# Performance work log

Measured on AMD Instinct MI355X. Metric: run time of the kernel, lower is better.

The kernel has to match this reference:

```python
import jax, jax.numpy as jnp
import numpy as np

NU, NI = 100000, 50000
N = NU + NI
CU, CI = 100, 100
D = 64
NL = 3
NNZ = 4_000_000
CNNZ = 5000
B = 4096


def setup_inputs() -> dict:
    key = jax.random.key(0)
    ks = jax.random.split(key, 24)
    def edges(k1, k2, k3, nnz, n):
        return (jax.random.randint(k1, (nnz,), 0, n, dtype=jnp.int32),
                jax.random.randint(k2, (nnz,), 0, n, dtype=jnp.int32),
                jax.random.uniform(k3, (nnz,), dtype=jnp.float32) * 0.05)
    ar, ac, av = edges(ks[0], ks[1], ks[2], NNZ, N)
    s1r, s1c, s1v = edges(ks[3], ks[4], ks[5], NNZ, N)
    s2r, s2c, s2v = edges(ks[6], ks[7], ks[8], NNZ, N)
    cr, cc, cv = edges(ks[9], ks[10], ks[11], CNNZ, CU + CI)
    return {
        "user_emb": jax.random.normal(ks[12], (NU, D), dtype=jnp.float32) * 0.1,
        "item_emb": jax.random.normal(ks[13], (NI, D), dtype=jnp.float32) * 0.1,
        "adj_rows": ar, "adj_cols": ac, "adj_vals": av,
        "sg1_rows": s1r, "sg1_cols": s1c, "sg1_vals": s1v,
        "sg2_rows": s2r, "sg2_cols": s2c, "sg2_vals": s2v,
        "uc": jax.random.uniform(ks[14], (NU, CU), dtype=jnp.float32),
        "ic": jax.random.uniform(ks[15], (NI, CI), dtype=jnp.float32),
        "cg_rows": cr, "cg_cols": cc, "cg_vals": cv,
        "users": jax.random.randint(ks[16], (B,), 0, NU, dtype=jnp.int32),
        "items": jax.random.randint(ks[17], (B,), 0, NI, dtype=jnp.int32),
        "neg_items": jax.random.randint(ks[18], (B,), 0, NI, dtype=jnp.int32),
    }


def _gcn(rows, cols, vals, ego, n):
    """n_layers of SpMM propagation + mean over layer outputs (incl. layer 0)."""
    acc = ego
    x = ego
    for _ in range(NL):
        x = jax.ops.segment_sum(vals[:, None] * x[cols], rows, num_segments=n)
        acc = acc + x
    return acc / (NL + 1)


def reference(user_emb, item_emb,
              adj_rows, adj_cols, adj_vals,
              sg1_rows, sg1_cols, sg1_vals,
              sg2_rows, sg2_cols, sg2_vals,
              uc, ic, cg_rows, cg_cols, cg_vals,
              users, items, neg_items):
    ego = jnp.concatenate([user_emb, item_emb], axis=0)  # [N, D]
    e0 = _gcn(adj_rows, adj_cols, adj_vals, ego, N)
    e1 = _gcn(sg1_rows, sg1_cols, sg1_vals, ego, N)
    e2 = _gcn(sg2_rows, sg2_cols, sg2_vals, ego, N)
    # community GCN: project node embeddings onto community space, propagate, lift back
    ucf = uc.T @ user_emb                                # [CU, D]
    icf = ic.T @ item_emb                                # [CI, D]
    ec = _gcn(cg_rows, cg_cols, cg_vals,
              jnp.concatenate([ucf, icf], axis=0), CU + CI)
    u3 = uc @ ec[:CU]                                    # [NU, D]
    i3 = ic @ ec[CU:]                                    # [NI, D]
    user_f = jnp.concatenate([e0[:NU], e1[:NU], e2[:NU], u3], axis=1)  # [NU, 4D]
    item_f = jnp.concatenate([e0[NU:], e1[NU:], e2[NU:], i3], axis=1)  # [NI, 4D]
    ue = user_f[users]
    ie = item_f[items]
    ne = item_f[neg_items]
    # sup_logits = <u, i_pos> - <u, i_neg>
    return jnp.sum(ue * (ie - ne), axis=-1)
```

## Files before the change

kernel.cpp:

```cpp
#include <hip/hip_runtime.h>
#include <hip/hip_fp16.h>
#include <cstdint>
#include <cstddef>

#define NU_ 100000
#define NI_ 50000
#define NN_ 150000
#define D_  64
#define NNZ_ 4000000
#define CN_ 200
#define CNNZ_ 5000
#define B_ 4096

#define NB2   512
#define RPB2  293
#define SLICE 40
#define NBLK  512
#define ECAP  8448

#define NP    4
#define COLP  37500
#define HSZ   (RPB2 * NP)

#define PROJB 1024

#define VSC_   256.0f

#if defined(__has_builtin)
#if __has_builtin(__builtin_amdgcn_cvt_scalef32_pk_f32_fp4) && \
    __has_builtin(__builtin_amdgcn_cvt_scalef32_pk_fp4_f32)
#define USE_FP4 1
#endif
#endif
#ifndef USE_FP4
#define USE_FP4 0
#endif

#if USE_FP4
#define FSC0 8.0f
#define FSC1 32.0f
#define FSC2 512.0f
#define ROWB 32
#else
#define FSC0 32.0f
#define FSC1 32.0f
#define FSC2 32.0f
#define ROWB 64
#endif

typedef float v2f __attribute__((ext_vector_type(2)));
typedef int   v4i __attribute__((ext_vector_type(4)));
typedef float v4f __attribute__((ext_vector_type(4)));

__device__ __forceinline__ float cv8(unsigned char b) {
    return __builtin_amdgcn_cvt_f32_fp8((int)b, 0);
}


#if USE_FP4
__global__ __launch_bounds__(256) void k_toq(const float* __restrict__ a,
                                             const float* __restrict__ b,
                                             unsigned* __restrict__ dst) {
    size_t gid = (size_t)blockIdx.x * 256 + threadIdx.x;
    size_t off = gid * 8;
    if (off >= (size_t)NN_ * D_) return;
    const float* src = (off < (size_t)NU_ * D_) ? a + off : b + (off - (size_t)NU_ * D_);
    float4 f0 = *(const float4*)src;
    float4 f1 = *(const float4*)(src + 4);
    unsigned w = 0;
    w = __builtin_amdgcn_cvt_scalef32_pk_fp4_f32(w, f0.x * FSC0, f0.y * FSC0, 1.0f, 0);
    w = __builtin_amdgcn_cvt_scalef32_pk_fp4_f32(w, f0.z * FSC0, f0.w * FSC0, 1.0f, 1);
    w = __builtin_amdgcn_cvt_scalef32_pk_fp4_f32(w, f1.x * FSC0, f1.y * FSC0, 1.0f, 2);
    w = __builtin_amdgcn_cvt_scalef32_pk_fp4_f32(w, f1.z * FSC0, f1.w * FSC0, 1.0f, 3);
    dst[gid] = w;
}
#else
__global__ __launch_bounds__(256) void k_toq(const float* __restrict__ a,
                                             const float* __restrict__ b,
                                             unsigned* __restrict__ dst) {
    size_t gid = (size_t)blockIdx.x * 256 + threadIdx.x;
    size_t off = gid * 4;
    if (off >= (size_t)NN_ * D_) return;
    const float* src = (off < (size_t)NU_ * D_) ? a + off : b + (off - (size_t)NU_ * D_);
    float4 f = *(const float4*)src;
    int p = 0;
    p = __builtin_amdgcn_cvt_pk_fp8_f32(f.x * FSC0, f.y * FSC0, p, false);
    p = __builtin_amdgcn_cvt_pk_fp8_f32(f.z * FSC0, f.w * FSC0, p, true);
    dst[gid] = (unsigned)p;
}
#endif


__global__ __launch_bounds__(256) void k_bin(const int* __restrict__ rows,
                                             const int* __restrict__ cols,
                                             const float* __restrict__ vals,
                                             int* __restrict__ bcnt,
                                             int2* __restrict__ gbuf) {
    __shared__ int lcur[NB2];
    int t = threadIdx.x;
    for (int i = t; i < NB2; i += 256) lcur[i] = 0;
    __syncthreads();
    size_t blockbase = (size_t)blockIdx.x * NB2 * SLICE;

    for (int base = blockIdx.x * 1024; base < NNZ_; base += gridDim.x * 1024) {
        int i0 = base + t * 4;
        if (i0 < NNZ_) {
            v4i r4 = __builtin_nontemporal_load((const v4i*)(rows + i0));
            v4i c4 = __builtin_nontemporal_load((const v4i*)(cols + i0));
            v4f v4 = __builtin_nontemporal_load((const v4f*)(vals + i0));
            #pragma unroll
            for (int k = 0; k < 4; k++) {
                int r = (k == 0) ? r4.x : (k == 1) ? r4.y : (k == 2) ? r4.z : r4.w;
                int c = (k == 0) ? c4.x : (k == 1) ? c4.y : (k == 2) ? c4.z : c4.w;
                float v = (k == 0) ? v4.x : (k == 1) ? v4.y : (k == 2) ? v4.z : v4.w;
                int b  = r / RPB2;
                int rl = r - b * RPB2;
                int pos = atomicAdd(&lcur[b], 1);
                if (pos < SLICE)
                    gbuf[blockbase + (size_t)b * SLICE + pos] =
                        make_int2((rl << 18) | c, __float_as_int(v));
            }
        }
    }
    __syncthreads();
    for (int i = t; i < NB2; i += 256)
        bcnt[(size_t)blockIdx.x * NB2 + i] = min(lcur[i], SLICE);
}


__global__ void k_btot(const int* __restrict__ bcnt, int* __restrict__ btot) {
    __shared__ int s[256];
    int b = blockIdx.x, t = threadIdx.x;
    int sum = 0;
    for (int sl = t; sl < NBLK; sl += 256) sum += bcnt[(size_t)sl * NB2 + b];
    s[t] = sum;
    __syncthreads();
    for (int o = 128; o > 0; o >>= 1) {
        if (t < o) s[t] += s[t + o];
        __syncthreads();
    }
    if (t == 0) btot[b] = s[0];
}

__global__ void k_bscan(const int* __restrict__ btot, int* __restrict__ bbase,
                        int* __restrict__ row_ptr) {
    __shared__ int s[NB2];
    int t = threadIdx.x;
    int v = btot[t];
    s[t] = v;
    __syncthreads();
    for (int o = 1; o < NB2; o <<= 1) {
        int x = (t >= o) ? s[t - o] : 0;
        __syncthreads();
        s[t] += x;
        __syncthreads();
    }
    bbase[t] = s[t] - v;
    if (t == NB2 - 1) row_ptr[NN_] = s[t];
}


__global__ __launch_bounds__(1024) void k_csr(const int* __restrict__ bcnt,
                                              const int2* __restrict__ gbuf,
                                              const int* __restrict__ bbase,
                                              const int* __restrict__ btot,
                                              int* __restrict__ row_ptr,
                                              unsigned* __restrict__ ep) {
    __shared__ int h[HSZ];
    __shared__ int hx[HSZ];
    __shared__ int aux[1024];
    __shared__ unsigned estage[ECAP];
    int b = blockIdx.x, t = threadIdx.x;
    for (int i = t; i < HSZ; i += 1024) h[i] = 0;
    __syncthreads();

    int sl = t >> 1, part = t & 1;
    int n = bcnt[(size_t)sl * NB2 + b];
    const int2* src = gbuf + ((size_t)sl * NB2 + b) * SLICE;

    for (int i = part; i < n; i += 2) {
        unsigned xv = *(const unsigned*)(src + i);
        int rl = xv >> 18;
        int pnl = (int)(xv & 0x3FFFFu) / COLP;
        atomicAdd(&h[rl * NP + pnl], 1);
    }
    __syncthreads();

    int a0 = (2 * t     < HSZ) ? h[2 * t]     : 0;
    int a1 = (2 * t + 1 < HSZ) ? h[2 * t + 1] : 0;
    aux[t] = a0 + a1;
    __syncthreads();
    for (int o = 1; o < 1024; o <<= 1) {
        int x = (t >= o) ? aux[t - o] : 0;
        __syncthreads();
        aux[t] += x;
        __syncthreads();
    }
    int excl = t ? aux[t - 1] : 0;
    if (2 * t     < HSZ) hx[2 * t]     = excl;
    if (2 * t + 1 < HSZ) hx[2 * t + 1] = excl + a0;
    __syncthreads();

    int base = bbase[b];
    int r0 = b * RPB2;
    int rows_b = min(RPB2, NN_ - r0);
    for (int i = t; i < rows_b; i += 1024) row_ptr[r0 + i] = base + hx[i * NP];
    __syncthreads();

    for (int i = part; i < n; i += 2) {
        int2 e = src[i];
        unsigned ex = (unsigned)e.x;
        int rl = ex >> 18;
        unsigned c = ex & 0x3FFFFu;
        int pnl = (int)c / COLP;
        float v = __int_as_float(e.y) * VSC_;
        unsigned v8 = (unsigned)__builtin_amdgcn_cvt_pk_fp8_f32(v, 0.f, 0, false) & 0xFFu;
        int pos = atomicAdd(&hx[rl * NP + pnl], 1);
        if (pos < ECAP) estage[pos] = c | (v8 << 24);
    }
    __syncthreads();

    int total = btot[b];
    if (total > ECAP) total = ECAP;
    for (int i = t; i < total; i += 1024) ep[base + i] = estage[i];
}


__global__ __launch_bounds__(256) void k_spmm(const int* __restrict__ rp,
                                              const unsigned* __restrict__ ep,
                                              const unsigned char* __restrict__ xq,
                                              float finsc,
                                              unsigned char* __restrict__ xn) {
    int w = (blockIdx.x * 256 + threadIdx.x) >> 6;
    if (w >= NN_) return;
    int lane = threadIdx.x & 63;
    int oct = lane >> 3;
    int l8  = lane & 7;
    int j0 = rp[w], j1 = rp[w + 1];
    v2f a01 = {0.f, 0.f}, a23 = {0.f, 0.f}, a45 = {0.f, 0.f}, a67 = {0.f, 0.f};
    #pragma unroll 4
    for (int j = j0; j < j1; j += 8) {
        int je = j + oct;
        unsigned e = (je < j1) ? ep[je] : 0u;
        float v = __builtin_amdgcn_cvt_f32_fp8((int)e, 3);
        v2f vv = {v, v};
#if USE_FP4
        unsigned raw = *(const unsigned*)(xq + (size_t)(e & 0x3FFFFu) * 32 + l8 * 4);
        a01 += vv * __builtin_amdgcn_cvt_scalef32_pk_f32_fp4(raw, 1.0f, 0);
        a23 += vv * __builtin_amdgcn_cvt_scalef32_pk_f32_fp4(raw, 1.0f, 1);
        a45 += vv * __builtin_amdgcn_cvt_scalef32_pk_f32_fp4(raw, 1.0f, 2);
        a67 += vv * __builtin_amdgcn_cvt_scalef32_pk_f32_fp4(raw, 1.0f, 3);
#else
        uint2 raw = *(const uint2*)(xq + (size_t)(e & 0x3FFFFu) * 64 + l8 * 8);
        a01 += vv * __builtin_amdgcn_cvt_pk_f32_fp8((int)raw.x, false);
        a23 += vv * __builtin_amdgcn_cvt_pk_f32_fp8((int)raw.x, true);
        a45 += vv * __builtin_amdgcn_cvt_pk_f32_fp8((int)raw.y, false);
        a67 += vv * __builtin_amdgcn_cvt_pk_f32_fp8((int)raw.y, true);
#endif
    }
    float d0 = a01[0], d1 = a01[1], d2 = a23[0], d3 = a23[1];
    float d4 = a45[0], d5 = a45[1], d6 = a67[0], d7 = a67[1];
    #pragma unroll
    for (int o = 32; o >= 8; o >>= 1) {
        d0 += __shfl_xor(d0, o, 64); d1 += __shfl_xor(d1, o, 64);
        d2 += __shfl_xor(d2, o, 64); d3 += __shfl_xor(d3, o, 64);
        d4 += __shfl_xor(d4, o, 64); d5 += __shfl_xor(d5, o, 64);
        d6 += __shfl_xor(d6, o, 64); d7 += __shfl_xor(d7, o, 64);
    }
    if (lane < 8) {
#if USE_FP4
        unsigned o2 = 0;
        o2 = __builtin_amdgcn_cvt_scalef32_pk_fp4_f32(o2, d0 * finsc, d1 * finsc, 1.0f, 0);
        o2 = __builtin_amdgcn_cvt_scalef32_pk_fp4_f32(o2, d2 * finsc, d3 * finsc, 1.0f, 1);
        o2 = __builtin_amdgcn_cvt_scalef32_pk_fp4_f32(o2, d4 * finsc, d5 * finsc, 1.0f, 2);
        o2 = __builtin_amdgcn_cvt_scalef32_pk_fp4_f32(o2, d6 * finsc, d7 * finsc, 1.0f, 3);
        *(unsigned*)(xn + (size_t)w * 32 + l8 * 4) = o2;
#else
        int p0 = 0, p1 = 0;
        p0 = __builtin_amdgcn_cvt_pk_fp8_f32(d0 * finsc, d1 * finsc, p0, false);
        p0 = __builtin_amdgcn_cvt_pk_fp8_f32(d2 * finsc, d3 * finsc, p0, true);
        p1 = __builtin_amdgcn_cvt_pk_fp8_f32(d4 * finsc, d5 * finsc, p1, false);
        p1 = __builtin_amdgcn_cvt_pk_fp8_f32(d6 * finsc, d7 * finsc, p1, true);
        uint2 o2; o2.x = (unsigned)p0; o2.y = (unsigned)p1;
        *(uint2*)(xn + (size_t)w * 64 + l8 * 8) = o2;
#endif
    }
}


__global__ __launch_bounds__(256) void k_spmm_s(const int* __restrict__ rp,
                                                const unsigned* __restrict__ ep,
                                                const unsigned char* __restrict__ xq,
                                                float finsc,
                                                const int* __restrict__ users,
                                                const int* __restrict__ items,
                                                const int* __restrict__ negs,
                                                float* __restrict__ x3s) {
    int s = (blockIdx.x * 256 + threadIdx.x) >> 6;
    if (s >= 3 * B_) return;
    int lane = threadIdx.x & 63;
    int oct = lane >> 3;
    int l8  = lane & 7;
    int node;
    if (s < B_)          node = users[s];
    else if (s < 2 * B_) node = NU_ + items[s - B_];
    else                 node = NU_ + negs[s - 2 * B_];
    int j0 = rp[node], j1 = rp[node + 1];
    v2f a01 = {0.f, 0.f}, a23 = {0.f, 0.f}, a45 = {0.f, 0.f}, a67 = {0.f, 0.f};
    #pragma unroll 2
    for (int j = j0; j < j1; j += 8) {
        int je = j + oct;
        unsigned e = (je < j1) ? ep[je] : 0u;
        float v = __builtin_amdgcn_cvt_f32_fp8((int)e, 3);
        v2f vv = {v, v};
#if USE_FP4
        unsigned raw = *(const unsigned*)(xq + (size_t)(e & 0x3FFFFu) * 32 + l8 * 4);
        a01 += vv * __builtin_amdgcn_cvt_scalef32_pk_f32_fp4(raw, 1.0f, 0);
        a23 += vv * __builtin_amdgcn_cvt_scalef32_pk_f32_fp4(raw, 1.0f, 1);
        a45 += vv * __builtin_amdgcn_cvt_scalef32_pk_f32_fp4(raw, 1.0f, 2);
        a67 += vv * __builtin_amdgcn_cvt_scalef32_pk_f32_fp4(raw, 1.0f, 3);
#else
        uint2 raw = *(const uint2*)(xq + (size_t)(e & 0x3FFFFu) * 64 + l8 * 8);
        a01 += vv * __builtin_amdgcn_cvt_pk_f32_fp8((int)raw.x, false);
        a23 += vv * __builtin_amdgcn_cvt_pk_f32_fp8((int)raw.x, true);
        a45 += vv * __builtin_amdgcn_cvt_pk_f32_fp8((int)raw.y, false);
        a67 += vv * __builtin_amdgcn_cvt_pk_f32_fp8((int)raw.y, true);
#endif
    }
    float d0 = a01[0], d1 = a01[1], d2 = a23[0], d3 = a23[1];
    float d4 = a45[0], d5 = a45[1], d6 = a67[0], d7 = a67[1];
    #pragma unroll
    for (int o = 32; o >= 8; o >>= 1) {
        d0 += __shfl_xor(d0, o, 64); d1 += __shfl_xor(d1, o, 64);
        d2 += __shfl_xor(d2, o, 64); d3 += __shfl_xor(d3, o, 64);
        d4 += __shfl_xor(d4, o, 64); d5 += __shfl_xor(d5, o, 64);
        d6 += __shfl_xor(d6, o, 64); d7 += __shfl_xor(d7, o, 64);
    }
    if (lane < 8) {
        float* dst = x3s + (size_t)s * D_ + l8 * 8;
        *(float4*)dst       = make_float4(d0 * finsc, d1 * finsc, d2 * finsc, d3 * finsc);
        *(float4*)(dst + 4) = make_float4(d4 * finsc, d5 * finsc, d6 * finsc, d7 * finsc);
    }
}


__device__ __forceinline__ float ldq(const unsigned char* x, size_t row, int lane, float inv) {
#if USE_FP4
    unsigned byte = x[row * 32 + (lane >> 1)];
    v2f pr = __builtin_amdgcn_cvt_scalef32_pk_f32_fp4(byte, 1.0f, 0);
    return ((lane & 1) ? pr[1] : pr[0]) * inv;
#else
    return cv8(x[row * 64 + lane]) * inv;
#endif
}

template<bool FIRST>
__global__ void k_dot_graph(const float* __restrict__ ue, const float* __restrict__ ie,
                            const unsigned char* __restrict__ x1,
                            const unsigned char* __restrict__ x2,
                            const float* __restrict__ x3s,
                            const int* __restrict__ users, const int* __restrict__ items,
                            const int* __restrict__ negs, float* __restrict__ out) {
    int w = (blockIdx.x * blockDim.x + threadIdx.x) >> 6;
    int lane = threadIdx.x & 63;
    if (w >= B_) return;
    int u = users[w], ip = items[w], in_ = negs[w];
    const float i1 = 1.0f / FSC1, i2 = 1.0f / FSC2;
    size_t ru = (size_t)u, ri = (size_t)(NU_ + ip), rn = (size_t)(NU_ + in_);
    float du = ue[(size_t)u * D_ + lane]
             + ldq(x1, ru, lane, i1) + ldq(x2, ru, lane, i2) + x3s[(size_t)w * D_ + lane];
    float di = ie[(size_t)ip * D_ + lane]
             + ldq(x1, ri, lane, i1) + ldq(x2, ri, lane, i2) + x3s[(size_t)(B_ + w) * D_ + lane];
    float dn = ie[(size_t)in_ * D_ + lane]
             + ldq(x1, rn, lane, i1) + ldq(x2, rn, lane, i2) + x3s[(size_t)(2 * B_ + w) * D_ + lane];
    float p = du * (di - dn);
    for (int o = 32; o > 0; o >>= 1) p += __shfl_xor(p, o, 64);
    if (lane == 0) {
        if (FIRST) out[w] = p * 0.0625f;
        else       out[w] += p * 0.0625f;
    }
}


__global__ __launch_bounds__(256) void k_proj(const float* __restrict__ mat,
                                              const float* __restrict__ emb,
                                              int n, float* __restrict__ pbuf) {
    __shared__ float se[8 * 64];
    __shared__ float sc[8 * 100];
    int t = threadIdx.x;
    int d = t & 63, c0 = t >> 6;
    float a[25];
    #pragma unroll
    for (int k = 0; k < 25; k++) a[k] = 0.f;

    int upb = (n + gridDim.x - 1) / gridDim.x;
    int u0 = blockIdx.x * upb;
    int u1 = min(u0 + upb, n);
    int ub = u0;
    for (; ub + 8 <= u1; ub += 8) {
        const float4* e4 = (const float4*)(emb + (size_t)ub * 64);
        const float4* c4 = (const float4*)(mat + (size_t)ub * 100);
        float4* se4 = (float4*)se;
        float4* sc4 = (float4*)sc;
        for (int idx = t; idx < 328; idx += 256) {
            if (idx < 128) se4[idx] = e4[idx];
            else           sc4[idx - 128] = c4[idx - 128];
        }
        __syncthreads();
        #pragma unroll
        for (int ul = 0; ul < 8; ++ul) {
            float ev = se[(ul << 6) + d];
            #pragma unroll
            for (int k = 0; k < 25; k++)
                a[k] += sc[ul * 100 + c0 + (k << 2)] * ev;
        }
        __syncthreads();
    }
    if (ub < u1) {
        int m = u1 - ub;
        for (int idx = t; idx < m * 64; idx += 256) se[idx] = emb[(size_t)ub * 64 + idx];
        for (int idx = t; idx < m * 100; idx += 256) sc[idx] = mat[(size_t)ub * 100 + idx];
        __syncthreads();
        for (int ul = 0; ul < m; ++ul) {
            float ev = se[(ul << 6) + d];
            #pragma unroll
            for (int k = 0; k < 25; k++)
                a[k] += sc[ul * 100 + c0 + (k << 2)] * ev;
        }
    }
    float* dst = pbuf + (size_t)blockIdx.x * 6400;
    #pragma unroll
    for (int k = 0; k < 25; k++)
        dst[t + (k << 8)] = a[k];
}

__global__ __launch_bounds__(256) void k_preduce(const float* __restrict__ pbuf,
                                                 float* __restrict__ dst) {
    int e = blockIdx.x * 256 + threadIdx.x;
    const float* src = pbuf + (size_t)blockIdx.y * 128 * 6400 + e;
    float s = 0.f;
    #pragma unroll 8
    for (int p = 0; p < 128; p++) s += src[(size_t)p * 6400];
    atomicAdd(&dst[e], s);
}


__global__ void k_cspmm(const int* __restrict__ r, const int* __restrict__ c,
                        const float* __restrict__ v, const float* __restrict__ x,
                        float* __restrict__ xn) {
    int w = (blockIdx.x * blockDim.x + threadIdx.x) >> 6;
    int lane = threadIdx.x & 63;
    if (w >= CNNZ_) return;
    int rr = r[w], cc = c[w];
    float vv = v[w];
    atomicAdd(&xn[rr * 64 + lane], vv * x[cc * 64 + lane]);
}


__global__ void k_dot_comm(const float* __restrict__ uc, const float* __restrict__ ic,
                           const float* __restrict__ cego, const float* __restrict__ cb1,
                           const float* __restrict__ cb2, const float* __restrict__ cb3,
                           const int* __restrict__ users, const int* __restrict__ items,
                           const int* __restrict__ negs, float* __restrict__ out) {
    int w = (blockIdx.x * blockDim.x + threadIdx.x) >> 6;
    int lane = threadIdx.x & 63;
    if (w >= B_) return;
    int u = users[w], ip = items[w], in_ = negs[w];
    float u3 = 0.f, i3p = 0.f, i3n = 0.f;
    for (int cc = 0; cc < 100; ++cc) {
        int eu = cc * 64 + lane, ei = (100 + cc) * 64 + lane;
        float evU = cego[eu] + cb1[eu] + cb2[eu] + cb3[eu];
        float evI = cego[ei] + cb1[ei] + cb2[ei] + cb3[ei];
        u3  += uc[(size_t)u * 100 + cc] * evU;
        i3p += ic[(size_t)ip * 100 + cc] * evI;
        i3n += ic[(size_t)in_ * 100 + cc] * evI;
    }
    float p = u3 * (i3p - i3n);
    for (int o = 32; o > 0; o >>= 1) p += __shfl_xor(p, o, 64);
    if (lane == 0) out[w] += p * 0.0625f;
}


static inline char* alignp(char*& p, size_t bytes) {
    char* r = p;
    p += (bytes + 255) & ~(size_t)255;
    return r;
}

extern "C" void kernel_launch(void* const* d_in, const int* in_sizes, int n_in,
                              void* d_out, int out_size, void* d_ws, size_t ws_size,
                              hipStream_t stream) {
    const float* uemb = (const float*)d_in[0];
    const float* iemb = (const float*)d_in[1];
    const float* uc   = (const float*)d_in[11];
    const float* ic   = (const float*)d_in[12];
    const int*   cgr  = (const int*)d_in[13];
    const int*   cgc  = (const int*)d_in[14];
    const float* cgv  = (const float*)d_in[15];
    const int*   users = (const int*)d_in[16];
    const int*   items = (const int*)d_in[17];
    const int*   negs  = (const int*)d_in[18];
    float* out = (float*)d_out;

    char* p = (char*)d_ws;
    char*  A      = alignp(p, (size_t)NBLK * NB2 * SLICE * 8);
    unsigned char* egoq = (unsigned char*)alignp(p, (size_t)NN_ * 64);
    unsigned* ep  = (unsigned*)alignp(p, (size_t)NNZ_ * 4);
    float* x3s    = (float*)alignp(p, (size_t)3 * B_ * D_ * 4);
    int*   row_ptr= (int*)  alignp(p, (size_t)(NN_ + 1) * 4);
    int*   bcnt   = (int*)  alignp(p, (size_t)NBLK * NB2 * 4);
    int*   btot   = (int*)  alignp(p, NB2 * 4);
    int*   bbase  = (int*)  alignp(p, NB2 * 4);
    float* cego   = (float*)alignp(p, (size_t)CN_ * D_ * 4);
    float* cbs    = (float*)alignp(p, (size_t)3 * CN_ * D_ * 4);
    float* cb1 = cbs, *cb2 = cbs + CN_ * D_, *cb3 = cbs + 2 * CN_ * D_;

    int2*          gbuf = (int2*)A;
    unsigned char* xq1  = (unsigned char*)A;
    unsigned char* xq2  = (unsigned char*)(A + (size_t)NN_ * ROWB);
    float*         pbuf = (float*)A;

    const int gSp = (NN_ * 64) / 256;
    const int gS3 = (3 * B_ * 64) / 256;
    const int gB  = (B_ * 64) / 256;
    const int gC  = (CNNZ_ * 64) / 256;
#if USE_FP4
    const int gTQ = (NN_ * D_ / 8 + 255) / 256;
#else
    const int gTQ = (NN_ * D_ / 4 + 255) / 256;
#endif

    k_toq<<<gTQ, 256, 0, stream>>>(uemb, iemb, (unsigned*)egoq);

    const float fin1 = FSC1 / (256.0f * FSC0);
    const float fin2 = FSC2 / (256.0f * FSC1);
    const float fin3 = 1.0f / (256.0f * FSC2);

    for (int g = 0; g < 3; ++g) {
        const int*   rows = (const int*)d_in[2 + g * 3];
        const int*   cols = (const int*)d_in[3 + g * 3];
        const float* vals = (const float*)d_in[4 + g * 3];

        k_bin  <<<NBLK, 256, 0, stream>>>(rows, cols, vals, bcnt, gbuf);
        k_btot <<<NB2, 256, 0, stream>>>(bcnt, btot);
        k_bscan<<<1, NB2, 0, stream>>>(btot, bbase, row_ptr);
        k_csr  <<<NB2, 1024, 0, stream>>>(bcnt, gbuf, bbase, btot, row_ptr, ep);

        k_spmm<<<gSp, 256, 0, stream>>>(row_ptr, ep, egoq, fin1, xq1);
        k_spmm<<<gSp, 256, 0, stream>>>(row_ptr, ep, xq1,  fin2, xq2);
        k_spmm_s<<<gS3, 256, 0, stream>>>(row_ptr, ep, xq2, fin3, users, items, negs, x3s);

        if (g == 0)
            k_dot_graph<true ><<<gB, 256, 0, stream>>>(uemb, iemb, xq1, xq2, x3s,
                                                       users, items, negs, out);
        else
            k_dot_graph<false><<<gB, 256, 0, stream>>>(uemb, iemb, xq1, xq2, x3s,
                                                       users, items, negs, out);
    }

    hipMemsetAsync(cego, 0, (size_t)CN_ * D_ * 4, stream);
    k_proj<<<PROJB, 256, 0, stream>>>(uc, uemb, NU_, pbuf);
    k_preduce<<<dim3(25, 8), 256, 0, stream>>>(pbuf, cego);
    k_proj<<<PROJB, 256, 0, stream>>>(ic, iemb, NI_, pbuf);
    k_preduce<<<dim3(25, 8), 256, 0, stream>>>(pbuf, cego + 100 * 64);

    hipMemsetAsync(cbs, 0, (size_t)3 * CN_ * D_ * 4, stream);
    k_cspmm<<<gC, 256, 0, stream>>>(cgr, cgc, cgv, cego, cb1);
    k_cspmm<<<gC, 256, 0, stream>>>(cgr, cgc, cgv, cb1, cb2);
    k_cspmm<<<gC, 256, 0, stream>>>(cgr, cgc, cgv, cb2, cb3);

    k_dot_comm<<<gB, 256, 0, stream>>>(uc, ic, cego, cb1, cb2, cb3,
                                       users, items, negs, out);
}
```

Measured before the change: 873.2 us.

## Use fixed per-bucket CSR offsets to drop global count and scan kernels

Each row bucket now writes its edges at a fixed offset b*ECAP and keeps its own row_ptr segment of RPB2+1 entries, so no global exclusive scan over bucket totals is needed. This removes the k_btot and k_bscan launches for each of the three graphs. The SpMM kernels find a row's pointers with a divide by RPB2. The edge buffer grows to NB2*ECAP entries, so reads are spread over a sparser, padded array.

```diff
diff --git a/kernel.cpp b/kernel.cpp
--- a/kernel.cpp
+++ b/kernel.cpp
@@ -14,8 +14,8 @@
 
 #define NB2   512
 #define RPB2  293
+#define NBLK  512
 #define SLICE 40
-#define NBLK  512
 #define ECAP  8448
 
 #define NP    4
@@ -128,42 +128,8 @@
 }
 
 
-__global__ void k_btot(const int* __restrict__ bcnt, int* __restrict__ btot) {
-    __shared__ int s[256];
-    int b = blockIdx.x, t = threadIdx.x;
-    int sum = 0;
-    for (int sl = t; sl < NBLK; sl += 256) sum += bcnt[(size_t)sl * NB2 + b];
-    s[t] = sum;
-    __syncthreads();
-    for (int o = 128; o > 0; o >>= 1) {
-        if (t < o) s[t] += s[t + o];
-        __syncthreads();
-    }
-    if (t == 0) btot[b] = s[0];
-}
-
-__global__ void k_bscan(const int* __restrict__ btot, int* __restrict__ bbase,
-                        int* __restrict__ row_ptr) {
-    __shared__ int s[NB2];
-    int t = threadIdx.x;
-    int v = btot[t];
-    s[t] = v;
-    __syncthreads();
-    for (int o = 1; o < NB2; o <<= 1) {
-        int x = (t >= o) ? s[t - o] : 0;
-        __syncthreads();
-        s[t] += x;
-        __syncthreads();
-    }
-    bbase[t] = s[t] - v;
-    if (t == NB2 - 1) row_ptr[NN_] = s[t];
-}
-
-
 __global__ __launch_bounds__(1024) void k_csr(const int* __restrict__ bcnt,
                                               const int2* __restrict__ gbuf,
-                                              const int* __restrict__ bbase,
-                                              const int* __restrict__ btot,
                                               int* __restrict__ row_ptr,
                                               unsigned* __restrict__ ep) {
     __shared__ int h[HSZ];
@@ -201,10 +167,12 @@
     if (2 * t + 1 < HSZ) hx[2 * t + 1] = excl + a0;
     __syncthreads();
 
-    int base = bbase[b];
+    int base = b * ECAP;
     int r0 = b * RPB2;
     int rows_b = min(RPB2, NN_ - r0);
-    for (int i = t; i < rows_b; i += 1024) row_ptr[r0 + i] = base + hx[i * NP];
+    int* rpb = row_ptr + (size_t)b * (RPB2 + 1);
+    for (int i = t; i < rows_b; i += 1024) rpb[i] = base + hx[i * NP];
+    if (t == 0) rpb[rows_b] = base + min(aux[1023], ECAP);
     __syncthreads();
 
     for (int i = part; i < n; i += 2) {
@@ -220,7 +188,7 @@
     }
     __syncthreads();
 
-    int total = btot[b];
+    int total = aux[1023];
     if (total > ECAP) total = ECAP;
     for (int i = t; i < total; i += 1024) ep[base + i] = estage[i];
 }
@@ -236,7 +204,10 @@
     int lane = threadIdx.x & 63;
     int oct = lane >> 3;
     int l8  = lane & 7;
-    int j0 = rp[w], j1 = rp[w + 1];
+    int bb = w / RPB2;
+    int rl = w - bb * RPB2;
+    const int* rpb = rp + (size_t)bb * (RPB2 + 1) + rl;
+    int j0 = rpb[0], j1 = rpb[1];
     v2f a01 = {0.f, 0.f}, a23 = {0.f, 0.f}, a45 = {0.f, 0.f}, a67 = {0.f, 0.f};
     #pragma unroll 4
     for (int j = j0; j < j1; j += 8) {
@@ -305,7 +276,10 @@
     if (s < B_)          node = users[s];
     else if (s < 2 * B_) node = NU_ + items[s - B_];
     else                 node = NU_ + negs[s - 2 * B_];
-    int j0 = rp[node], j1 = rp[node + 1];
+    int bb = node / RPB2;
+    int rl = node - bb * RPB2;
+    const int* rpb = rp + (size_t)bb * (RPB2 + 1) + rl;
+    int j0 = rpb[0], j1 = rpb[1];
     v2f a01 = {0.f, 0.f}, a23 = {0.f, 0.f}, a45 = {0.f, 0.f}, a67 = {0.f, 0.f};
     #pragma unroll 2
     for (int j = j0; j < j1; j += 8) {
@@ -505,12 +479,10 @@
     char* p = (char*)d_ws;
     char*  A      = alignp(p, (size_t)NBLK * NB2 * SLICE * 8);
     unsigned char* egoq = (unsigned char*)alignp(p, (size_t)NN_ * 64);
-    unsigned* ep  = (unsigned*)alignp(p, (size_t)NNZ_ * 4);
+    unsigned* ep  = (unsigned*)alignp(p, (size_t)NB2 * ECAP * 4);
     float* x3s    = (float*)alignp(p, (size_t)3 * B_ * D_ * 4);
-    int*   row_ptr= (int*)  alignp(p, (size_t)(NN_ + 1) * 4);
+    int*   row_ptr= (int*)  alignp(p, (size_t)NB2 * (RPB2 + 1) * 4);
     int*   bcnt   = (int*)  alignp(p, (size_t)NBLK * NB2 * 4);
-    int*   btot   = (int*)  alignp(p, NB2 * 4);
-    int*   bbase  = (int*)  alignp(p, NB2 * 4);
     float* cego   = (float*)alignp(p, (size_t)CN_ * D_ * 4);
     float* cbs    = (float*)alignp(p, (size_t)3 * CN_ * D_ * 4);
     float* cb1 = cbs, *cb2 = cbs + CN_ * D_, *cb3 = cbs + 2 * CN_ * D_;
@@ -541,10 +513,8 @@
         const int*   cols = (const int*)d_in[3 + g * 3];
         const float* vals = (const float*)d_in[4 + g * 3];
 
-        k_bin  <<<NBLK, 256, 0, stream>>>(rows, cols, vals, bcnt, gbuf);
-        k_btot <<<NB2, 256, 0, stream>>>(bcnt, btot);
-        k_bscan<<<1, NB2, 0, stream>>>(btot, bbase, row_ptr);
-        k_csr  <<<NB2, 1024, 0, stream>>>(bcnt, gbuf, bbase, btot, row_ptr, ep);
+        k_bin<<<NBLK, 256, 0, stream>>>(rows, cols, vals, bcnt, gbuf);
+        k_csr<<<NB2, 1024, 0, stream>>>(bcnt, gbuf, row_ptr, ep);
 
         k_spmm<<<gSp, 256, 0, stream>>>(row_ptr, ep, egoq, fin1, xq1);
         k_spmm<<<gSp, 256, 0, stream>>>(row_ptr, ep, xq1,  fin2, xq2);
```

Result: faster. 853.6 us (-2.2%).
